# Kernel tuning notes

Hardware: AMD Instinct MI355X
Metric: run time of the kernel (lower is better)

Reference implementation:

```python
import jax, jax.numpy as jnp
import numpy as np

B, S, T = 8, 2048, 128  # batch, seq_len, token_embedding_dim (== dep_transformed_dim, required by source bug)


def setup_inputs() -> dict:
    key = jax.random.key(0)
    k1, k2, k3, k4, k5, k6, k7 = jax.random.split(key, 7)
    sT = 1.0 / np.sqrt(T)
    sS = 1.0 / np.sqrt(S)
    return {
        "token_embeddings": jax.random.normal(k1, (B, S, T), jnp.float32),
        "dep_embeddings": jax.random.normal(k2, (B, S, T), jnp.float32),  # dead input (source bug), kept for fidelity
        "dep_heads": jax.random.randint(k3, (B, S), 0, S, jnp.int32),
        # composition_transform = Bilinear(T, T, T): weight [T_out, T_in1, T_in2], bias [T_out]
        "W_comp": jax.random.uniform(k4, (T, T, T), jnp.float32, -sT, sT),
        "b_comp": jax.random.uniform(k5, (T,), jnp.float32, -sT, sT),
        # reduction_transform = Linear(S, 1)
        "w_red": jax.random.uniform(k6, (1, S), jnp.float32, -sS, sS),
        "b_red": jax.random.uniform(k7, (1,), jnp.float32, -sS, sS),
    }


def reference(token_embeddings, dep_embeddings, dep_heads, W_comp, b_comp, w_red, b_red):
    # Faithful to source semantics (including the bug where dep_transform output is
    # discarded and tanh is applied to token_embeddings instead):
    #   dense[b,i,j,:] = tanh( bilinear(token[b,j], mask(i==heads[b,j]) * tanh(token[b,j])) )
    #   out[b,i,t]     = sum_j w_red[j] * dense[b,i,j,t] + b_red
    # Where mask is zero, bilinear collapses to its bias, so we never materialize
    # the [B,S,S,T] tensor: compute the 'active' value per token j and scatter-add
    # the delta vs. the bias-only baseline into row i = dep_heads[b,j].
    h = jnp.tanh(token_embeddings)                                   # [B,S,T]
    val = jnp.einsum('bsp,tpq,bsq->bst', token_embeddings, W_comp, h) + b_comp  # [B,S,T]
    act = jnp.tanh(val)                                              # active (masked-in) values
    base_val = jnp.tanh(b_comp)                                      # [T] value where mask is zero
    w = w_red[0]                                                     # [S], reduction weights over j
    base = jnp.sum(w) * base_val + b_red[0]                          # [T] bias-only row
    delta = w[None, :, None] * (act - base_val)                      # [B,S,T]
    b_idx = jnp.arange(token_embeddings.shape[0])[:, None]           # [B,1]
    out = base + jnp.zeros_like(act).at[b_idx, dep_heads].add(delta) # scatter over head rows
    return out
```

## Files before the change

kernel.cpp:

```cpp
#include <hip/hip_runtime.h>
#include <hip/hip_fp16.h>
#include <math.h>

#define S_LEN 2048
#define T_DIM 128
#define BM 128
#define TN 64
#define NBLK 256
#define TOKR 132

typedef _Float16 half8 __attribute__((ext_vector_type(8)));
typedef _Float16 half4t __attribute__((ext_vector_type(4)));
typedef float floatx16 __attribute__((ext_vector_type(16)));

__device__ __forceinline__ float tanh_fast(float x) {
  return 1.0f - __fdividef(2.0f, 1.0f + __expf(2.0f * x));
}

__global__ __launch_bounds__(256) void prep_kernel(
    const float* __restrict__ W, const float* __restrict__ w_red,
    const float* __restrict__ b_comp, const float* __restrict__ b_red,
    _Float16* __restrict__ W16f, float* __restrict__ out) {
  const int blk = blockIdx.x;
  const int tid = threadIdx.x;
  if (blk < 1024) {
    const int t = blk >> 3;
    const int qh = (blk >> 2) & 1;
    const int it = blk & 3;
    const int tc = t >> 5, tl = t & 31;
    const int e8 = it * 256 + tid;
    const int p = e8 >> 3;
    const int q = qh * 64 + (e8 & 7) * 8;
    const float* src = W + (size_t)t * 16384 + (size_t)p * 128 + q;
    const float4 v0 = *(const float4*)src;
    const float4 v1 = *(const float4*)(src + 4);
    half8 h;
    h[0] = (_Float16)v0.x; h[1] = (_Float16)v0.y;
    h[2] = (_Float16)v0.z; h[3] = (_Float16)v0.w;
    h[4] = (_Float16)v1.x; h[5] = (_Float16)v1.y;
    h[6] = (_Float16)v1.z; h[7] = (_Float16)v1.w;
    const int kc = q >> 4, lh2 = (q >> 3) & 1;
    *(half8*)(W16f + ((size_t)((p * 4 + tc) * 8 + kc)) * 512 + lh2 * 256 + tl * 8) = h;
  } else {
    __shared__ float red4[4];
    float part = 0.f;
#pragma unroll
    for (int i = 0; i < 8; ++i) part += w_red[tid * 8 + i];
#pragma unroll
    for (int off = 32; off > 0; off >>= 1) part += __shfl_down(part, off, 64);
    if ((tid & 63) == 0) red4[tid >> 6] = part;
    __syncthreads();
    const float Sw = red4[0] + red4[1] + red4[2] + red4[3];
    const float br = b_red[0];
    const size_t base = (size_t)(blk - 1024) * 1024 + (size_t)tid * 4;
    const int t0 = (int)(base & 127);
    float4 v;
    v.x = Sw * tanh_fast(b_comp[t0 + 0]) + br;
    v.y = Sw * tanh_fast(b_comp[t0 + 1]) + br;
    v.z = Sw * tanh_fast(b_comp[t0 + 2]) + br;
    v.w = Sw * tanh_fast(b_comp[t0 + 3]) + br;
    *(float4*)(out + base) = v;
  }
}

__global__ __launch_bounds__(512, 2) void main_kernel(
    const float* __restrict__ tok, const int* __restrict__ heads,
    const _Float16* __restrict__ W16f, const float* __restrict__ b_comp,
    const float* __restrict__ w_red, float* __restrict__ out) {
  __shared__ _Float16 tokT2[128 * TOKR];
  __shared__ float red[2][BM * TN];

  const int tid = threadIdx.x;
  const int lane = tid & 63;
  const int kh = tid >> 6;
  const int l31 = lane & 31;
  const int lh = lane >> 5;
  const int blk = blockIdx.x;
  const int th = blk & 1;
  const int mb = blk >> 1;
  const int pstag = ((blk >> 3) * 4) & 127;
  const size_t tokbase = (size_t)mb * BM * T_DIM;

#pragma unroll
  for (int it = 0; it < 8; ++it) {
    const int f = it * 512 + tid;
    const int m = f >> 5;
    const int p0 = (f & 31) * 4;
    const float4 v = *(const float4*)(tok + tokbase + (size_t)m * 128 + p0);
    const int mi = (m & 31) * 4 + (m >> 5);
    const float vv[4] = {v.x, v.y, v.z, v.w};
#pragma unroll
    for (int jj = 0; jj < 4; ++jj) {
      const int p = p0 + jj;
      const int col = mi ^ (((p + (p >> 3)) & 7) << 2);
      tokT2[p * TOKR + col] = (_Float16)vv[jj];
    }
  }

  half8 h16[4];
#pragma unroll
  for (int mh = 0; mh < 4; ++mh) {
    const int m = mh * 32 + l31;
    const int q0 = kh * 16 + lh * 8;
    const float4 v0 = *(const float4*)(tok + tokbase + (size_t)m * 128 + q0);
    const float4 v1 = *(const float4*)(tok + tokbase + (size_t)m * 128 + q0 + 4);
    h16[mh][0] = (_Float16)tanh_fast(v0.x);
    h16[mh][1] = (_Float16)tanh_fast(v0.y);
    h16[mh][2] = (_Float16)tanh_fast(v0.z);
    h16[mh][3] = (_Float16)tanh_fast(v0.w);
    h16[mh][4] = (_Float16)tanh_fast(v1.x);
    h16[mh][5] = (_Float16)tanh_fast(v1.y);
    h16[mh][6] = (_Float16)tanh_fast(v1.z);
    h16[mh][7] = (_Float16)tanh_fast(v1.w);
  }

  int off[2];
#pragma unroll
  for (int tt = 0; tt < 2; ++tt)
    off[tt] = (((th * 2 + tt) * 8 + kh) << 9) + lane * 8;

  half8 bf0[2], bf1[2], bf2[2];
  half4t tk0, tk1, tk2;

  auto loadB = [&](half8 (&bf)[2], int p) {
    const int pp = (p + pstag) & 127;
    const _Float16* wp = W16f + (size_t)pp * 16384;
    bf[0] = *(const half8*)(wp + off[0]);
    bf[1] = *(const half8*)(wp + off[1]);
  };
  auto loadT = [&](half4t& tk, int p) {
    const int pp = (p + pstag) & 127;
    const int col = (l31 * 4) ^ (((pp + (pp >> 3)) & 7) << 2);
    tk = *(const half4t*)(tokT2 + pp * TOKR + col);
  };

  loadB(bf0, 0);
  loadB(bf1, 1);

  floatx16 acc[4][2];
#pragma unroll
  for (int mh = 0; mh < 4; ++mh)
#pragma unroll
    for (int tt = 0; tt < 2; ++tt)
#pragma unroll
      for (int r = 0; r < 16; ++r) acc[mh][tt][r] = 0.f;

  __syncthreads();

  auto compute = [&](half8 (&bf)[2], half4t tk) {
#pragma unroll
    for (int mh = 0; mh < 4; ++mh) {
      half8 a = h16[mh] * tk[mh];
      acc[mh][0] = __builtin_amdgcn_mfma_f32_32x32x16_f16(a, bf[0], acc[mh][0], 0, 0, 0);
      acc[mh][1] = __builtin_amdgcn_mfma_f32_32x32x16_f16(a, bf[1], acc[mh][1], 0, 0, 0);
    }
  };

  loadT(tk0, 0);
  loadT(tk1, 1);
  for (int p = 0; p < 126; p += 3) {
    loadB(bf2, p + 2);  loadT(tk2, p + 2);
    compute(bf0, tk0);
    loadB(bf0, p + 3);  loadT(tk0, p + 3);
    compute(bf1, tk1);
    loadB(bf1, p + 4);  loadT(tk1, p + 4);
    compute(bf2, tk2);
  }
  compute(bf0, tk0);
  compute(bf1, tk1);

  __syncthreads();
  {
    float* R = &red[kh & 1][0];
    const int g = kh >> 1;
#pragma unroll
    for (int phase = 0; phase < 4; ++phase) {
      if (g == phase) {
#pragma unroll
        for (int mh = 0; mh < 4; ++mh)
#pragma unroll
          for (int tt = 0; tt < 2; ++tt) {
            const int t_loc = tt * 32 + l31;
#pragma unroll
            for (int r = 0; r < 16; ++r) {
              const int m_loc = mh * 32 + (r & 3) + 8 * (r >> 2) + 4 * lh;
              const int addr = m_loc * TN + t_loc;
              if (phase == 0) R[addr] = acc[mh][tt][r];
              else            R[addr] += acc[mh][tt][r];
            }
          }
      }
      __syncthreads();
    }
  }

  const int t_loc = tid & 63;
  const int mgrp = tid >> 6;
  const int t = th * 64 + t_loc;
  const float bc = b_comp[t];
  const float tb = tanh_fast(bc);
#pragma unroll 4
  for (int mi = 0; mi < 16; ++mi) {
    const int m_loc = mi * 8 + mgrp;
    const int gm = mb * BM + m_loc;
    const int head = heads[gm];
    const float wr = w_red[gm & 2047];
    const float v = red[0][m_loc * TN + t_loc] + red[1][m_loc * TN + t_loc] + bc;
    atomicAdd(out + ((size_t)(gm >> 11) * S_LEN + head) * T_DIM + t,
              wr * (tanh_fast(v) - tb));
  }
}

extern "C" void kernel_launch(void* const* d_in, const int* in_sizes, int n_in,
                              void* d_out, int out_size, void* d_ws, size_t ws_size,
                              hipStream_t stream) {
  const float* tok    = (const float*)d_in[0];
  const int*   heads  = (const int*)d_in[2];
  const float* W      = (const float*)d_in[3];
  const float* b_comp = (const float*)d_in[4];
  const float* w_red  = (const float*)d_in[5];
  const float* b_red  = (const float*)d_in[6];
  float* out = (float*)d_out;

  _Float16* W16f = (_Float16*)d_ws;

  prep_kernel<<<3072, 256, 0, stream>>>(W, w_red, b_comp, b_red, W16f, out);
  main_kernel<<<NBLK, 512, 0, stream>>>(tok, heads, W16f, b_comp, w_red, out);
}
```

Baseline: 151.6 us.

## Stream fp16 weight tiles into an LDS ring via async global_load_lds

Replaces the register-based triple-buffered global loads of the fp16 weight fragments with asynchronous global-to-LDS loads into a per-wave 6-slot ring, tracked with s_waitcnt vmcnt. Each substep reads the next fragment from LDS while computing the current MFMAs, then issues the load six steps ahead. The goal is to hide global-memory latency and free the VGPRs used for prefetching. In exchange it enlarges the shared-memory footprint and reuses that space for the reduction buffers. The reuse is risky because loads past the end of the loop may still be in flight, so they could overwrite the reduction buffers unless the barrier drains them.

```diff
diff --git a/kernel.cpp b/kernel.cpp
--- a/kernel.cpp
+++ b/kernel.cpp
@@ -8,14 +8,25 @@
 #define TN 64
 #define NBLK 256
 #define TOKR 132
+#define RING_OFF 34816
+#define SLOT_B 2048
 
 typedef _Float16 half8 __attribute__((ext_vector_type(8)));
 typedef _Float16 half4t __attribute__((ext_vector_type(4)));
 typedef float floatx16 __attribute__((ext_vector_type(16)));
+typedef unsigned int u32;
 
 __device__ __forceinline__ float tanh_fast(float x) {
   return 1.0f - __fdividef(2.0f, 1.0f + __expf(2.0f * x));
 }
+
+__device__ __forceinline__ void load_lds16(const void* g, void* l) {
+  __builtin_amdgcn_global_load_lds(
+      (const __attribute__((address_space(1))) u32*)g,
+      (__attribute__((address_space(3))) u32*)l, 16, 0, 0);
+}
+
+#define VM() asm volatile("s_waitcnt vmcnt(8)" ::: "memory")
 
 __global__ __launch_bounds__(256) void prep_kernel(
     const float* __restrict__ W, const float* __restrict__ w_red,
@@ -67,8 +78,10 @@
     const float* __restrict__ tok, const int* __restrict__ heads,
     const _Float16* __restrict__ W16f, const float* __restrict__ b_comp,
     const float* __restrict__ w_red, float* __restrict__ out) {
-  __shared__ _Float16 tokT2[128 * TOKR];
-  __shared__ float red[2][BM * TN];
+  __shared__ __align__(16) char smem[133120];
+  _Float16* const tokT2 = (_Float16*)smem;
+  float* const red0 = (float*)smem;
+  float* const red1 = (float*)smem + BM * TN;
 
   const int tid = threadIdx.x;
   const int lane = tid & 63;
@@ -80,6 +93,30 @@
   const int mb = blk >> 1;
   const int pstag = ((blk >> 3) * 4) & 127;
   const size_t tokbase = (size_t)mb * BM * T_DIM;
+
+  char* const ringp = smem + RING_OFF + kh * (6 * SLOT_B);
+  const char* const wsrc0 =
+      (const char*)W16f + (size_t)(th * 2 + 0) * 8192 + kh * 1024 + lane * 16;
+  const char* const wsrc1 =
+      (const char*)W16f + (size_t)(th * 2 + 1) * 8192 + kh * 1024 + lane * 16;
+
+  auto issue = [&](int step, int slot) {
+    const size_t pb = (size_t)((step + pstag) & 127) * 32768;
+    load_lds16(wsrc0 + pb, ringp + slot * SLOT_B);
+    load_lds16(wsrc1 + pb, ringp + slot * SLOT_B + 1024);
+  };
+  auto readF = [&](half8 (&bf)[2], int slot) {
+    bf[0] = *(const half8*)(ringp + slot * SLOT_B + lane * 16);
+    bf[1] = *(const half8*)(ringp + slot * SLOT_B + 1024 + lane * 16);
+  };
+  auto readT = [&](half4t& tk, int step) {
+    const int pp = (step + pstag) & 127;
+    const int col = (l31 * 4) ^ (((pp + (pp >> 3)) & 7) << 2);
+    tk = *(const half4t*)(tokT2 + pp * TOKR + col);
+  };
+
+#pragma unroll
+  for (int s = 0; s < 6; ++s) issue(s, s);
 
 #pragma unroll
   for (int it = 0; it < 8; ++it) {
@@ -114,29 +151,6 @@
     h16[mh][7] = (_Float16)tanh_fast(v1.w);
   }
 
-  int off[2];
-#pragma unroll
-  for (int tt = 0; tt < 2; ++tt)
-    off[tt] = (((th * 2 + tt) * 8 + kh) << 9) + lane * 8;
-
-  half8 bf0[2], bf1[2], bf2[2];
-  half4t tk0, tk1, tk2;
-
-  auto loadB = [&](half8 (&bf)[2], int p) {
-    const int pp = (p + pstag) & 127;
-    const _Float16* wp = W16f + (size_t)pp * 16384;
-    bf[0] = *(const half8*)(wp + off[0]);
-    bf[1] = *(const half8*)(wp + off[1]);
-  };
-  auto loadT = [&](half4t& tk, int p) {
-    const int pp = (p + pstag) & 127;
-    const int col = (l31 * 4) ^ (((pp + (pp >> 3)) & 7) << 2);
-    tk = *(const half4t*)(tokT2 + pp * TOKR + col);
-  };
-
-  loadB(bf0, 0);
-  loadB(bf1, 1);
-
   floatx16 acc[4][2];
 #pragma unroll
   for (int mh = 0; mh < 4; ++mh)
@@ -156,22 +170,35 @@
     }
   };
 
-  loadT(tk0, 0);
-  loadT(tk1, 1);
-  for (int p = 0; p < 126; p += 3) {
-    loadB(bf2, p + 2);  loadT(tk2, p + 2);
-    compute(bf0, tk0);
-    loadB(bf0, p + 3);  loadT(tk0, p + 3);
-    compute(bf1, tk1);
-    loadB(bf1, p + 4);  loadT(tk1, p + 4);
-    compute(bf2, tk2);
-  }
-  compute(bf0, tk0);
-  compute(bf1, tk1);
+  half8 bfA[2], bfB[2];
+  half4t tkA, tkB;
+  readF(bfA, 0);  readT(tkA, 0);
+
+#define SUBSTEP(s, BFC, TKC, BFN, TKN)      \
+  {                                         \
+    VM();                                   \
+    readF(BFN, (s + 1) % 6);                \
+    readT(TKN, P + s + 1);                  \
+    compute(BFC, TKC);                      \
+    issue(P + s + 6, s);                    \
+  }
+  for (int P = 0; P < 126; P += 6) {
+    SUBSTEP(0, bfA, tkA, bfB, tkB);
+    SUBSTEP(1, bfB, tkB, bfA, tkA);
+    SUBSTEP(2, bfA, tkA, bfB, tkB);
+    SUBSTEP(3, bfB, tkB, bfA, tkA);
+    SUBSTEP(4, bfA, tkA, bfB, tkB);
+    SUBSTEP(5, bfB, tkB, bfA, tkA);
+  }
+#undef SUBSTEP
+  VM();
+  readF(bfB, 1);  readT(tkB, 127);
+  compute(bfA, tkA);
+  compute(bfB, tkB);
 
   __syncthreads();
   {
-    float* R = &red[kh & 1][0];
+    float* R = (kh & 1) ? red1 : red0;
     const int g = kh >> 1;
 #pragma unroll
     for (int phase = 0; phase < 4; ++phase) {
@@ -205,7 +232,7 @@
     const int gm = mb * BM + m_loc;
     const int head = heads[gm];
     const float wr = w_red[gm & 2047];
-    const float v = red[0][m_loc * TN + t_loc] + red[1][m_loc * TN + t_loc] + bc;
+    const float v = red0[m_loc * TN + t_loc] + red1[m_loc * TN + t_loc] + bc;
     atomicAdd(out + ((size_t)(gm >> 11) * S_LEN + head) * T_DIM + t,
               wr * (tanh_fast(v) - tb));
   }
```

After: 153.1 us. About the same (+1.0%).

## Software-pipeline MFMA operand build, alias LDS buffers, add setprio around MFMAs

Applied to the files above, without the earlier changes.

Restructures the main loop so the scaled A fragments for the next step are built while the current step's MFMAs run, with two A buffers ping-ponged over a six-step unrolled loop. MFMA bursts are wrapped in s_setprio to favour the matrix issue. The token-transpose buffer and the reduction buffers now share one 64KB LDS allocation, and the first W loads are issued before the token staging. It also makes the w_red sum in the prep kernel read coalesced. The cost is more register pressure from the extra A buffers, and correctness depends on the barrier separating tokT2 reads from the red writes.

```diff
diff --git a/kernel.cpp b/kernel.cpp
--- a/kernel.cpp
+++ b/kernel.cpp
@@ -45,7 +45,7 @@
     __shared__ float red4[4];
     float part = 0.f;
 #pragma unroll
-    for (int i = 0; i < 8; ++i) part += w_red[tid * 8 + i];
+    for (int i = 0; i < 8; ++i) part += w_red[i * 256 + tid];
 #pragma unroll
     for (int off = 32; off > 0; off >>= 1) part += __shfl_down(part, off, 64);
     if ((tid & 63) == 0) red4[tid >> 6] = part;
@@ -67,8 +67,10 @@
     const float* __restrict__ tok, const int* __restrict__ heads,
     const _Float16* __restrict__ W16f, const float* __restrict__ b_comp,
     const float* __restrict__ w_red, float* __restrict__ out) {
-  __shared__ _Float16 tokT2[128 * TOKR];
-  __shared__ float red[2][BM * TN];
+  __shared__ __align__(16) char smem[65536];
+  _Float16* const tokT2 = (_Float16*)smem;
+  float* const red0 = (float*)smem;
+  float* const red1 = (float*)smem + BM * TN;
 
   const int tid = threadIdx.x;
   const int lane = tid & 63;
@@ -81,6 +83,35 @@
   const int pstag = ((blk >> 3) * 4) & 127;
   const size_t tokbase = (size_t)mb * BM * T_DIM;
 
+  int off[2];
+#pragma unroll
+  for (int tt = 0; tt < 2; ++tt)
+    off[tt] = (((th * 2 + tt) * 8 + kh) << 9) + lane * 8;
+
+  half8 bf0[2], bf1[2], bf2[2];
+  half4t tk0, tk1, tk2;
+  half8 aA[4], aB[4];
+  half8 h16[4];
+
+  auto loadB = [&](half8 (&bf)[2], int p) {
+    const int pp = (p + pstag) & 127;
+    const _Float16* wp = W16f + (size_t)pp * 16384;
+    bf[0] = *(const half8*)(wp + off[0]);
+    bf[1] = *(const half8*)(wp + off[1]);
+  };
+  auto loadT = [&](half4t& tk, int p) {
+    const int pp = (p + pstag) & 127;
+    const int col = (l31 * 4) ^ (((pp + (pp >> 3)) & 7) << 2);
+    tk = *(const half4t*)(tokT2 + pp * TOKR + col);
+  };
+  auto build = [&](half8 (&a)[4], half4t tk) {
+#pragma unroll
+    for (int mh = 0; mh < 4; ++mh) a[mh] = h16[mh] * tk[mh];
+  };
+
+  loadB(bf0, 0);
+  loadB(bf1, 1);
+
 #pragma unroll
   for (int it = 0; it < 8; ++it) {
     const int f = it * 512 + tid;
@@ -97,7 +128,6 @@
     }
   }
 
-  half8 h16[4];
 #pragma unroll
   for (int mh = 0; mh < 4; ++mh) {
     const int m = mh * 32 + l31;
@@ -114,29 +144,6 @@
     h16[mh][7] = (_Float16)tanh_fast(v1.w);
   }
 
-  int off[2];
-#pragma unroll
-  for (int tt = 0; tt < 2; ++tt)
-    off[tt] = (((th * 2 + tt) * 8 + kh) << 9) + lane * 8;
-
-  half8 bf0[2], bf1[2], bf2[2];
-  half4t tk0, tk1, tk2;
-
-  auto loadB = [&](half8 (&bf)[2], int p) {
-    const int pp = (p + pstag) & 127;
-    const _Float16* wp = W16f + (size_t)pp * 16384;
-    bf[0] = *(const half8*)(wp + off[0]);
-    bf[1] = *(const half8*)(wp + off[1]);
-  };
-  auto loadT = [&](half4t& tk, int p) {
-    const int pp = (p + pstag) & 127;
-    const int col = (l31 * 4) ^ (((pp + (pp >> 3)) & 7) << 2);
-    tk = *(const half4t*)(tokT2 + pp * TOKR + col);
-  };
-
-  loadB(bf0, 0);
-  loadB(bf1, 1);
-
   floatx16 acc[4][2];
 #pragma unroll
   for (int mh = 0; mh < 4; ++mh)
@@ -147,31 +154,43 @@
 
   __syncthreads();
 
-  auto compute = [&](half8 (&bf)[2], half4t tk) {
+  auto mfma8 = [&](half8 (&a)[4], half8 (&bf)[2]) {
+    __builtin_amdgcn_s_setprio(1);
 #pragma unroll
     for (int mh = 0; mh < 4; ++mh) {
-      half8 a = h16[mh] * tk[mh];
-      acc[mh][0] = __builtin_amdgcn_mfma_f32_32x32x16_f16(a, bf[0], acc[mh][0], 0, 0, 0);
-      acc[mh][1] = __builtin_amdgcn_mfma_f32_32x32x16_f16(a, bf[1], acc[mh][1], 0, 0, 0);
+      acc[mh][0] = __builtin_amdgcn_mfma_f32_32x32x16_f16(a[mh], bf[0], acc[mh][0], 0, 0, 0);
+      acc[mh][1] = __builtin_amdgcn_mfma_f32_32x32x16_f16(a[mh], bf[1], acc[mh][1], 0, 0, 0);
     }
+    __builtin_amdgcn_s_setprio(0);
   };
 
   loadT(tk0, 0);
   loadT(tk1, 1);
-  for (int p = 0; p < 126; p += 3) {
-    loadB(bf2, p + 2);  loadT(tk2, p + 2);
-    compute(bf0, tk0);
-    loadB(bf0, p + 3);  loadT(tk0, p + 3);
-    compute(bf1, tk1);
-    loadB(bf1, p + 4);  loadT(tk1, p + 4);
-    compute(bf2, tk2);
-  }
-  compute(bf0, tk0);
-  compute(bf1, tk1);
+  build(aA, tk0);
+
+#define SUBSTEP(BF_CUR, BF_PRE, TK_NXT, TK_PRE, A_CUR, A_NXT, K) \
+  {                                                              \
+    mfma8(A_CUR, BF_CUR);                                        \
+    loadB(BF_PRE, (K) + 2);                                      \
+    loadT(TK_PRE, (K) + 2);                                      \
+    build(A_NXT, TK_NXT);                                        \
+  }
+  for (int p = 0; p < 126; p += 6) {
+    SUBSTEP(bf0, bf2, tk1, tk2, aA, aB, p + 0);
+    SUBSTEP(bf1, bf0, tk2, tk0, aB, aA, p + 1);
+    SUBSTEP(bf2, bf1, tk0, tk1, aA, aB, p + 2);
+    SUBSTEP(bf0, bf2, tk1, tk2, aB, aA, p + 3);
+    SUBSTEP(bf1, bf0, tk2, tk0, aA, aB, p + 4);
+    SUBSTEP(bf2, bf1, tk0, tk1, aB, aA, p + 5);
+  }
+#undef SUBSTEP
+  mfma8(aA, bf0);
+  build(aB, tk1);
+  mfma8(aB, bf1);
 
   __syncthreads();
   {
-    float* R = &red[kh & 1][0];
+    float* R = (kh & 1) ? red1 : red0;
     const int g = kh >> 1;
 #pragma unroll
     for (int phase = 0; phase < 4; ++phase) {
@@ -205,7 +224,7 @@
     const int gm = mb * BM + m_loc;
     const int head = heads[gm];
     const float wr = w_red[gm & 2047];
-    const float v = red[0][m_loc * TN + t_loc] + red[1][m_loc * TN + t_loc] + bc;
+    const float v = red0[m_loc * TN + t_loc] + red1[m_loc * TN + t_loc] + bc;
     atomicAdd(out + ((size_t)(gm >> 11) * S_LEN + head) * T_DIM + t,
               wr * (tanh_fast(v) - tb));
   }
```

Result: no change. 151.0 us (-0.4%).

## Count head multiplicity to replace atomics with stores, overlap smem reduction planes

Applied to the files above, without the earlier changes.

The prep kernel now builds a per-row histogram of dep_heads, after a memset, and stores the sum of the reduction weights. In the main kernel, rows that receive exactly one contribution get a plain store of base plus delta instead of an atomicAdd. The cross-wave reduction now writes four planes of partial sums into shared memory aliased over the token tile, which cuts the phased passes from four barrier rounds to two. The W loads are also moved earlier to overlap with the token staging. It adds a memset launch and a global atomic histogram, and relies on the workspace being large enough.

```diff
diff --git a/kernel.cpp b/kernel.cpp
--- a/kernel.cpp
+++ b/kernel.cpp
@@ -20,7 +20,9 @@
 __global__ __launch_bounds__(256) void prep_kernel(
     const float* __restrict__ W, const float* __restrict__ w_red,
     const float* __restrict__ b_comp, const float* __restrict__ b_red,
-    _Float16* __restrict__ W16f, float* __restrict__ out) {
+    const int* __restrict__ heads,
+    _Float16* __restrict__ W16f, float* __restrict__ out,
+    int* counts, float* swslot) {
   const int blk = blockIdx.x;
   const int tid = threadIdx.x;
   if (blk < 1024) {
@@ -43,16 +45,22 @@
     *(half8*)(W16f + ((size_t)((p * 4 + tc) * 8 + kc)) * 512 + lh2 * 256 + tl * 8) = h;
   } else {
     __shared__ float red4[4];
+    const int blk2 = blk - 1024;
+    if (counts != nullptr && tid < 8) {
+      const int gm = blk2 * 8 + tid;
+      atomicAdd(&counts[(gm >> 11) * 2048 + heads[gm]], 1);
+    }
     float part = 0.f;
 #pragma unroll
-    for (int i = 0; i < 8; ++i) part += w_red[tid * 8 + i];
+    for (int i = 0; i < 8; ++i) part += w_red[i * 256 + tid];
 #pragma unroll
     for (int off = 32; off > 0; off >>= 1) part += __shfl_down(part, off, 64);
     if ((tid & 63) == 0) red4[tid >> 6] = part;
     __syncthreads();
     const float Sw = red4[0] + red4[1] + red4[2] + red4[3];
+    if (swslot != nullptr && blk2 == 0 && tid == 0) swslot[0] = Sw;
     const float br = b_red[0];
-    const size_t base = (size_t)(blk - 1024) * 1024 + (size_t)tid * 4;
+    const size_t base = (size_t)blk2 * 1024 + (size_t)tid * 4;
     const int t0 = (int)(base & 127);
     float4 v;
     v.x = Sw * tanh_fast(b_comp[t0 + 0]) + br;
@@ -66,9 +74,12 @@
 __global__ __launch_bounds__(512, 2) void main_kernel(
     const float* __restrict__ tok, const int* __restrict__ heads,
     const _Float16* __restrict__ W16f, const float* __restrict__ b_comp,
-    const float* __restrict__ w_red, float* __restrict__ out) {
-  __shared__ _Float16 tokT2[128 * TOKR];
-  __shared__ float red[2][BM * TN];
+    const float* __restrict__ w_red, const float* __restrict__ b_red,
+    const int* __restrict__ cnts, const float* __restrict__ swsl,
+    const int use_cnt, float* __restrict__ out) {
+  __shared__ __align__(16) char smem[131072];
+  _Float16* const tokT2 = (_Float16*)smem;
+  float* const planes = (float*)smem;
 
   const int tid = threadIdx.x;
   const int lane = tid & 63;
@@ -81,6 +92,30 @@
   const int pstag = ((blk >> 3) * 4) & 127;
   const size_t tokbase = (size_t)mb * BM * T_DIM;
 
+  int off[2];
+#pragma unroll
+  for (int tt = 0; tt < 2; ++tt)
+    off[tt] = (((th * 2 + tt) * 8 + kh) << 9) + lane * 8;
+
+  half8 bf0[2], bf1[2], bf2[2];
+  half4t tk0, tk1, tk2;
+  half8 h16[4];
+
+  auto loadB = [&](half8 (&bf)[2], int p) {
+    const int pp = (p + pstag) & 127;
+    const _Float16* wp = W16f + (size_t)pp * 16384;
+    bf[0] = *(const half8*)(wp + off[0]);
+    bf[1] = *(const half8*)(wp + off[1]);
+  };
+  auto loadT = [&](half4t& tk, int p) {
+    const int pp = (p + pstag) & 127;
+    const int col = (l31 * 4) ^ (((pp + (pp >> 3)) & 7) << 2);
+    tk = *(const half4t*)(tokT2 + pp * TOKR + col);
+  };
+
+  loadB(bf0, 0);
+  loadB(bf1, 1);
+
 #pragma unroll
   for (int it = 0; it < 8; ++it) {
     const int f = it * 512 + tid;
@@ -97,7 +132,6 @@
     }
   }
 
-  half8 h16[4];
 #pragma unroll
   for (int mh = 0; mh < 4; ++mh) {
     const int m = mh * 32 + l31;
@@ -114,29 +148,6 @@
     h16[mh][7] = (_Float16)tanh_fast(v1.w);
   }
 
-  int off[2];
-#pragma unroll
-  for (int tt = 0; tt < 2; ++tt)
-    off[tt] = (((th * 2 + tt) * 8 + kh) << 9) + lane * 8;
-
-  half8 bf0[2], bf1[2], bf2[2];
-  half4t tk0, tk1, tk2;
-
-  auto loadB = [&](half8 (&bf)[2], int p) {
-    const int pp = (p + pstag) & 127;
-    const _Float16* wp = W16f + (size_t)pp * 16384;
-    bf[0] = *(const half8*)(wp + off[0]);
-    bf[1] = *(const half8*)(wp + off[1]);
-  };
-  auto loadT = [&](half4t& tk, int p) {
-    const int pp = (p + pstag) & 127;
-    const int col = (l31 * 4) ^ (((pp + (pp >> 3)) & 7) << 2);
-    tk = *(const half4t*)(tokT2 + pp * TOKR + col);
-  };
-
-  loadB(bf0, 0);
-  loadB(bf1, 1);
-
   floatx16 acc[4][2];
 #pragma unroll
   for (int mh = 0; mh < 4; ++mh)
@@ -171,27 +182,36 @@
 
   __syncthreads();
   {
-    float* R = &red[kh & 1][0];
-    const int g = kh >> 1;
-#pragma unroll
-    for (int phase = 0; phase < 4; ++phase) {
-      if (g == phase) {
-#pragma unroll
-        for (int mh = 0; mh < 4; ++mh)
-#pragma unroll
-          for (int tt = 0; tt < 2; ++tt) {
-            const int t_loc = tt * 32 + l31;
-#pragma unroll
-            for (int r = 0; r < 16; ++r) {
-              const int m_loc = mh * 32 + (r & 3) + 8 * (r >> 2) + 4 * lh;
-              const int addr = m_loc * TN + t_loc;
-              if (phase == 0) R[addr] = acc[mh][tt][r];
-              else            R[addr] += acc[mh][tt][r];
-            }
+    float* P = planes + (kh >> 1) * (BM * TN);
+    const int ph = kh & 1;
+    if (ph == 0) {
+#pragma unroll
+      for (int mh = 0; mh < 4; ++mh)
+#pragma unroll
+        for (int tt = 0; tt < 2; ++tt) {
+          const int t_loc = tt * 32 + l31;
+#pragma unroll
+          for (int r = 0; r < 16; ++r) {
+            const int m_loc = mh * 32 + (r & 3) + 8 * (r >> 2) + 4 * lh;
+            P[m_loc * TN + t_loc] = acc[mh][tt][r];
           }
-      }
-      __syncthreads();
-    }
+        }
+    }
+    __syncthreads();
+    if (ph == 1) {
+#pragma unroll
+      for (int mh = 0; mh < 4; ++mh)
+#pragma unroll
+        for (int tt = 0; tt < 2; ++tt) {
+          const int t_loc = tt * 32 + l31;
+#pragma unroll
+          for (int r = 0; r < 16; ++r) {
+            const int m_loc = mh * 32 + (r & 3) + 8 * (r >> 2) + 4 * lh;
+            P[m_loc * TN + t_loc] += acc[mh][tt][r];
+          }
+        }
+    }
+    __syncthreads();
   }
 
   const int t_loc = tid & 63;
@@ -199,15 +219,26 @@
   const int t = th * 64 + t_loc;
   const float bc = b_comp[t];
   const float tb = tanh_fast(bc);
+  const float brv = b_red[0];
+  const float Swv = use_cnt ? swsl[0] : 0.f;
+  const float base_t = Swv * tb + brv;
 #pragma unroll 4
   for (int mi = 0; mi < 16; ++mi) {
     const int m_loc = mi * 8 + mgrp;
     const int gm = mb * BM + m_loc;
     const int head = heads[gm];
     const float wr = w_red[gm & 2047];
-    const float v = red[0][m_loc * TN + t_loc] + red[1][m_loc * TN + t_loc] + bc;
-    atomicAdd(out + ((size_t)(gm >> 11) * S_LEN + head) * T_DIM + t,
-              wr * (tanh_fast(v) - tb));
+    const int a = m_loc * TN + t_loc;
+    const float v = planes[a] + planes[BM * TN + a] + planes[2 * BM * TN + a] +
+                    planes[3 * BM * TN + a] + bc;
+    const float val = wr * (tanh_fast(v) - tb);
+    const int row = (gm >> 11) * 2048 + head;
+    float* dst = out + (size_t)row * T_DIM + t;
+    if (use_cnt && cnts[row] == 1) {
+      *dst = base_t + val;
+    } else {
+      atomicAdd(dst, val);
+    }
   }
 }
 
@@ -224,6 +255,16 @@
 
   _Float16* W16f = (_Float16*)d_ws;
 
-  prep_kernel<<<3072, 256, 0, stream>>>(W, w_red, b_comp, b_red, W16f, out);
-  main_kernel<<<NBLK, 512, 0, stream>>>(tok, heads, W16f, b_comp, w_red, out);
-}
+  const size_t W16_BYTES = 4u * 1024u * 1024u;
+  const size_t CNT_BYTES = 8u * 2048u * sizeof(int);
+  const size_t need = W16_BYTES + CNT_BYTES + 16;
+  const int use_cnt = (ws_size >= need) ? 1 : 0;
+  int*   counts = use_cnt ? (int*)((char*)d_ws + W16_BYTES) : nullptr;
+  float* swslot = use_cnt ? (float*)((char*)d_ws + W16_BYTES + CNT_BYTES) : nullptr;
+
+  if (use_cnt) hipMemsetAsync(counts, 0, CNT_BYTES, stream);
+  prep_kernel<<<3072, 256, 0, stream>>>(W, w_red, b_comp, b_red, heads,
+                                        W16f, out, counts, swslot);
+  main_kernel<<<NBLK, 512, 0, stream>>>(tok, heads, W16f, b_comp, w_red, b_red,
+                                        counts, swslot, use_cnt, out);
+}
```

Result: slower. 155.3 us (+2.4%).
